# Kernel tuning notes

Hardware: AMD Instinct MI355X
Metric: run time of the kernel (lower is better)

The kernel has to match this reference:

```python
import jax, jax.numpy as jnp
import numpy as np

IN_FEATURES = 512
OUT_FEATURES = 64
INTER = 16
BATCH = 512


def setup_inputs() -> dict:
    key = jax.random.key(0)
    kx, kt = jax.random.split(key)
    x = jax.random.normal(kx, (BATCH, IN_FEATURES), dtype=jnp.float32)
    T = jax.random.normal(kt, (IN_FEATURES, OUT_FEATURES * INTER), dtype=jnp.float32)
    return {"x": x, "T": T}


def reference(x, T):
    B = x.shape[0]
    # M: [B, out, inter]
    M = (x @ T).reshape(B, OUT_FEATURES, INTER)
    # pairwise L1 distance over the intermediate dim: [B, B, out]
    l1 = jnp.sum(jnp.abs(M[:, None, :, :] - M[None, :, :, :]), axis=3)
    sim = jnp.exp(-l1)
    mask = 1.0 - jnp.eye(B, dtype=x.dtype)[:, :, None]  # exclude self
    o_b = jnp.sum(sim * mask, axis=1)  # [B, out]
    return jnp.concatenate([x, o_b], axis=1)
```

## Files before the change

kernel.cpp:

```cpp
#include <hip/hip_runtime.h>

#define OUT_STRIDE 576

typedef __attribute__((ext_vector_type(8))) short bf16x8;
typedef __attribute__((ext_vector_type(4))) float f32x4;

__device__ inline unsigned short f2bf(float f) {
    unsigned u = __float_as_uint(f);
    u = (u + 0x7FFFu + ((u >> 16) & 1u)) >> 16;
    return (unsigned short)u;
}

__global__ __launch_bounds__(256) void transpose_T_kernel(
    const float* __restrict__ T, unsigned short* __restrict__ Tb)
{
    __shared__ float tt[64][68];
    const int b = blockIdx.x;
    const int t = threadIdx.x;
    const int k0 = (b & 7) * 64, n0 = (b >> 3) * 64;
    const int n4 = (t & 15) * 4, kr = t >> 4;
#pragma unroll
    for (int rr = 0; rr < 4; ++rr) {
        const int k = rr * 16 + kr;
        *(float4*)&tt[k][n4] = *(const float4*)(T + (size_t)(k0 + k) * 1024 + n0 + n4);
    }
    __syncthreads();
#pragma unroll
    for (int q = 0; q < 4; ++q) {
        const int g = q * 256 + t;
        const int nn = g >> 4, c = g & 15;
        ushort4 w;
        w.x = f2bf(tt[c * 4 + 0][nn]);
        w.y = f2bf(tt[c * 4 + 1][nn]);
        w.z = f2bf(tt[c * 4 + 2][nn]);
        w.w = f2bf(tt[c * 4 + 3][nn]);
        *(ushort4*)(Tb + (size_t)(n0 + nn) * 512 + k0 + c * 4) = w;
    }
}

__global__ __launch_bounds__(256) void gemm_kernel(
    const float* __restrict__ x, const unsigned short* __restrict__ Tb,
    float* __restrict__ M, float* __restrict__ out)
{
    __shared__ unsigned short As[32 * 72];
    __shared__ unsigned short Bs[64 * 72];
    const int t = threadIdx.x;
    const int bx = blockIdx.x & 15, by = blockIdx.x >> 4;
    const int c0 = bx * 64, r0 = by * 32;
    const int lane = t & 63, w = t >> 6;
    const int m0 = (w >> 1) * 16, nb = (w & 1) * 32;
    const int fl = lane & 15, q8 = (lane >> 4) * 8;
    const int arow = t >> 3, k8 = (t & 7) * 8;

    f32x4 acc0 = {0.f, 0.f, 0.f, 0.f}, acc1 = {0.f, 0.f, 0.f, 0.f};

    for (int kc = 0; kc < 512; kc += 64) {
        {
            const float4 u = *(const float4*)(x + (size_t)(r0 + arow) * 512 + kc + k8);
            const float4 v = *(const float4*)(x + (size_t)(r0 + arow) * 512 + kc + k8 + 4);
            ushort4 w0, w1;
            w0.x = f2bf(u.x); w0.y = f2bf(u.y); w0.z = f2bf(u.z); w0.w = f2bf(u.w);
            w1.x = f2bf(v.x); w1.y = f2bf(v.y); w1.z = f2bf(v.z); w1.w = f2bf(v.w);
            *(ushort4*)&As[arow * 72 + k8] = w0;
            *(ushort4*)&As[arow * 72 + k8 + 4] = w1;
        }
#pragma unroll
        for (int h = 0; h < 2; ++h) {
            const int n = arow + h * 32;
            *(uint4*)&Bs[n * 72 + k8] =
                *(const uint4*)(Tb + (size_t)(c0 + n) * 512 + kc + k8);
        }
        __syncthreads();
        const bf16x8 a0  = *(const bf16x8*)&As[(m0 + fl) * 72 + q8];
        const bf16x8 a1  = *(const bf16x8*)&As[(m0 + fl) * 72 + 32 + q8];
        const bf16x8 b00 = *(const bf16x8*)&Bs[(nb + fl) * 72 + q8];
        const bf16x8 b01 = *(const bf16x8*)&Bs[(nb + fl) * 72 + 32 + q8];
        const bf16x8 b10 = *(const bf16x8*)&Bs[(nb + 16 + fl) * 72 + q8];
        const bf16x8 b11 = *(const bf16x8*)&Bs[(nb + 16 + fl) * 72 + 32 + q8];
        acc0 = __builtin_amdgcn_mfma_f32_16x16x32_bf16(a0, b00, acc0, 0, 0, 0);
        acc0 = __builtin_amdgcn_mfma_f32_16x16x32_bf16(a1, b01, acc0, 0, 0, 0);
        acc1 = __builtin_amdgcn_mfma_f32_16x16x32_bf16(a0, b10, acc1, 0, 0, 0);
        acc1 = __builtin_amdgcn_mfma_f32_16x16x32_bf16(a1, b11, acc1, 0, 0, 0);
        __syncthreads();
    }
    const int orow = r0 + m0 + (lane >> 4) * 4;
#pragma unroll
    for (int r = 0; r < 4; ++r) {
        M[(size_t)(orow + r) * 1024 + c0 + nb + fl]      = acc0[r];
        M[(size_t)(orow + r) * 1024 + c0 + nb + 16 + fl] = acc1[r];
    }

    const int bid = blockIdx.x;
    {
        const int idx = (bid * 256 + t) * 4;
        const int i = idx >> 9, c = idx & 511;
        *(float4*)(out + (size_t)i * OUT_STRIDE + c) = *(const float4*)(x + idx);
    }
    if (t < 128) {
        const int idx = bid * 128 + t;
        const int i = idx >> 6, o = idx & 63;
        out[(size_t)i * OUT_STRIDE + 512 + o] = -1.0f;
    }
}

__global__ __launch_bounds__(256, 4) void pairwise_kernel(
    const float* __restrict__ M, float* __restrict__ out)
{
    __shared__ float sj[8 * 1280];
    const int t = threadIdx.x;
    const int o = t & 63, ig = t >> 6;
    const int it = blockIdx.x & 31, jc = blockIdx.x >> 5;
    const int i0 = it * 16, j0 = jc * 16;

    float mi[4][16];
#pragma unroll
    for (int r = 0; r < 4; ++r) {
        const float* rp = M + (size_t)(i0 + ig * 4 + r) * 1024 + o * 16;
#pragma unroll
        for (int q = 0; q < 4; ++q) {
            const float4 v = *(const float4*)(rp + q * 4);
            mi[r][q * 4 + 0] = v.x; mi[r][q * 4 + 1] = v.y;
            mi[r][q * 4 + 2] = v.z; mi[r][q * 4 + 3] = v.w;
        }
    }
    float acc[4] = {0.f, 0.f, 0.f, 0.f};

    const int os = t >> 2, k4 = t & 3;
#pragma unroll
    for (int jb = 0; jb < 16; jb += 8) {
#pragma unroll
        for (int q = 0; q < 8; ++q) {
            const float4 v = *(const float4*)(M + (size_t)(j0 + jb + q) * 1024 + t * 4);
            *(float4*)&sj[q * 1280 + os * 20 + k4 * 4] = v;
        }
        __syncthreads();
#pragma unroll
        for (int q = 0; q < 8; ++q) {
            const float* s = sj + q * 1280 + o * 20;
            float l1[4] = {0.f, 0.f, 0.f, 0.f};
#pragma unroll
            for (int q4 = 0; q4 < 4; ++q4) {
                const float4 v = *(const float4*)(s + q4 * 4);
#pragma unroll
                for (int r = 0; r < 4; ++r) {
                    l1[r] += fabsf(mi[r][q4 * 4 + 0] - v.x);
                    l1[r] += fabsf(mi[r][q4 * 4 + 1] - v.y);
                    l1[r] += fabsf(mi[r][q4 * 4 + 2] - v.z);
                    l1[r] += fabsf(mi[r][q4 * 4 + 3] - v.w);
                }
            }
#pragma unroll
            for (int r = 0; r < 4; ++r) acc[r] += __expf(-l1[r]);
        }
        __syncthreads();
    }
#pragma unroll
    for (int r = 0; r < 4; ++r)
        atomicAdd(out + (size_t)(i0 + ig * 4 + r) * OUT_STRIDE + 512 + o, acc[r]);
}

extern "C" void kernel_launch(void* const* d_in, const int* in_sizes, int n_in,
                              void* d_out, int out_size, void* d_ws, size_t ws_size,
                              hipStream_t stream) {
    const float* x = (const float*)d_in[0];
    const float* T = (const float*)d_in[1];
    float* out = (float*)d_out;
    float* M = (float*)d_ws;
    unsigned short* Tb = (unsigned short*)((char*)d_ws + (2 << 20));

    transpose_T_kernel<<<128, 256, 0, stream>>>(T, Tb);
    gemm_kernel<<<256, 256, 0, stream>>>(x, Tb, M, out);
    pairwise_kernel<<<1024, 256, 0, stream>>>(M, out);
}
```

Before: 83.86 us.

## Exploit L1 distance symmetry in pairwise kernel; split GEMM into smaller tiles

The pairwise kernel now visits only upper-triangular tile pairs (528 instead of 1024 blocks), mapping the block id to (ti,tj) with a sqrt-based triangular index. Each off-diagonal block also accumulates column sums and scatters them to the j rows through a shared-memory reduction and atomics, which roughly halves the exp and L1 work. In exchange it adds register pressure (16 extra accumulators, occupancy hint lowered from 4 to 3), an extra reduction pass and more atomics. The GEMM moves to 16-row tiles with twice as many blocks to spread work across more CUs.

Result: no change. 83.96 us (+0.1%).

```diff
diff --git a/kernel.cpp b/kernel.cpp
--- a/kernel.cpp
+++ b/kernel.cpp
@@ -42,75 +42,73 @@
     const float* __restrict__ x, const unsigned short* __restrict__ Tb,
     float* __restrict__ M, float* __restrict__ out)
 {
-    __shared__ unsigned short As[32 * 72];
+    __shared__ unsigned short As[16 * 72];
     __shared__ unsigned short Bs[64 * 72];
     const int t = threadIdx.x;
     const int bx = blockIdx.x & 15, by = blockIdx.x >> 4;
-    const int c0 = bx * 64, r0 = by * 32;
+    const int c0 = bx * 64, r0 = by * 16;
     const int lane = t & 63, w = t >> 6;
-    const int m0 = (w >> 1) * 16, nb = (w & 1) * 32;
+    const int nb = w * 16;
     const int fl = lane & 15, q8 = (lane >> 4) * 8;
-    const int arow = t >> 3, k8 = (t & 7) * 8;
+    const int ar = t >> 4, ak4 = (t & 15) * 4;
+    const int bn = t >> 3, bk8 = (t & 7) * 8;
 
-    f32x4 acc0 = {0.f, 0.f, 0.f, 0.f}, acc1 = {0.f, 0.f, 0.f, 0.f};
+    f32x4 acc = {0.f, 0.f, 0.f, 0.f};
 
     for (int kc = 0; kc < 512; kc += 64) {
         {
-            const float4 u = *(const float4*)(x + (size_t)(r0 + arow) * 512 + kc + k8);
-            const float4 v = *(const float4*)(x + (size_t)(r0 + arow) * 512 + kc + k8 + 4);
-            ushort4 w0, w1;
+            const float4 u = *(const float4*)(x + (size_t)(r0 + ar) * 512 + kc + ak4);
+            ushort4 w0;
             w0.x = f2bf(u.x); w0.y = f2bf(u.y); w0.z = f2bf(u.z); w0.w = f2bf(u.w);
-            w1.x = f2bf(v.x); w1.y = f2bf(v.y); w1.z = f2bf(v.z); w1.w = f2bf(v.w);
-            *(ushort4*)&As[arow * 72 + k8] = w0;
-            *(ushort4*)&As[arow * 72 + k8 + 4] = w1;
+            *(ushort4*)&As[ar * 72 + ak4] = w0;
         }
 #pragma unroll
         for (int h = 0; h < 2; ++h) {
-            const int n = arow + h * 32;
-            *(uint4*)&Bs[n * 72 + k8] =
-                *(const uint4*)(Tb + (size_t)(c0 + n) * 512 + kc + k8);
+            const int n = bn + h * 32;
+            *(uint4*)&Bs[n * 72 + bk8] =
+                *(const uint4*)(Tb + (size_t)(c0 + n) * 512 + kc + bk8);
         }
         __syncthreads();
-        const bf16x8 a0  = *(const bf16x8*)&As[(m0 + fl) * 72 + q8];
-        const bf16x8 a1  = *(const bf16x8*)&As[(m0 + fl) * 72 + 32 + q8];
-        const bf16x8 b00 = *(const bf16x8*)&Bs[(nb + fl) * 72 + q8];
-        const bf16x8 b01 = *(const bf16x8*)&Bs[(nb + fl) * 72 + 32 + q8];
-        const bf16x8 b10 = *(const bf16x8*)&Bs[(nb + 16 + fl) * 72 + q8];
-        const bf16x8 b11 = *(const bf16x8*)&Bs[(nb + 16 + fl) * 72 + 32 + q8];
-        acc0 = __builtin_amdgcn_mfma_f32_16x16x32_bf16(a0, b00, acc0, 0, 0, 0);
-        acc0 = __builtin_amdgcn_mfma_f32_16x16x32_bf16(a1, b01, acc0, 0, 0, 0);
-        acc1 = __builtin_amdgcn_mfma_f32_16x16x32_bf16(a0, b10, acc1, 0, 0, 0);
-        acc1 = __builtin_amdgcn_mfma_f32_16x16x32_bf16(a1, b11, acc1, 0, 0, 0);
+        const bf16x8 a0 = *(const bf16x8*)&As[fl * 72 + q8];
+        const bf16x8 a1 = *(const bf16x8*)&As[fl * 72 + 32 + q8];
+        const bf16x8 b0 = *(const bf16x8*)&Bs[(nb + fl) * 72 + q8];
+        const bf16x8 b1 = *(const bf16x8*)&Bs[(nb + fl) * 72 + 32 + q8];
+        acc = __builtin_amdgcn_mfma_f32_16x16x32_bf16(a0, b0, acc, 0, 0, 0);
+        acc = __builtin_amdgcn_mfma_f32_16x16x32_bf16(a1, b1, acc, 0, 0, 0);
         __syncthreads();
     }
-    const int orow = r0 + m0 + (lane >> 4) * 4;
+    const int orow = r0 + (lane >> 4) * 4;
 #pragma unroll
-    for (int r = 0; r < 4; ++r) {
-        M[(size_t)(orow + r) * 1024 + c0 + nb + fl]      = acc0[r];
-        M[(size_t)(orow + r) * 1024 + c0 + nb + 16 + fl] = acc1[r];
-    }
+    for (int r = 0; r < 4; ++r)
+        M[(size_t)(orow + r) * 1024 + c0 + nb + fl] = acc[r];
 
     const int bid = blockIdx.x;
-    {
-        const int idx = (bid * 256 + t) * 4;
+    if (t < 128) {
+        const int idx = (bid * 128 + t) * 4;
         const int i = idx >> 9, c = idx & 511;
         *(float4*)(out + (size_t)i * OUT_STRIDE + c) = *(const float4*)(x + idx);
-    }
-    if (t < 128) {
-        const int idx = bid * 128 + t;
+    } else if (t < 192) {
+        const int idx = bid * 64 + (t - 128);
         const int i = idx >> 6, o = idx & 63;
         out[(size_t)i * OUT_STRIDE + 512 + o] = -1.0f;
     }
 }
 
-__global__ __launch_bounds__(256, 4) void pairwise_kernel(
+__global__ __launch_bounds__(256, 3) void pairwise_kernel(
     const float* __restrict__ M, float* __restrict__ out)
 {
     __shared__ float sj[8 * 1280];
     const int t = threadIdx.x;
     const int o = t & 63, ig = t >> 6;
-    const int it = blockIdx.x & 31, jc = blockIdx.x >> 5;
-    const int i0 = it * 16, j0 = jc * 16;
+    const int b = blockIdx.x;
+
+    int ti = (int)((65.0f - sqrtf(4225.0f - 8.0f * (float)b)) * 0.5f);
+    if (b < ti * (65 - ti) / 2) --ti;
+    else if (b >= (ti + 1) * (64 - ti) / 2) ++ti;
+    const int st = ti * (65 - ti) / 2;
+    const int tj = ti + (b - st);
+    const int i0 = ti * 16, j0 = tj * 16;
+    const bool diag = (ti == tj);
 
     float mi[4][16];
 #pragma unroll
@@ -123,7 +121,10 @@
             mi[r][q * 4 + 2] = v.z; mi[r][q * 4 + 3] = v.w;
         }
     }
-    float acc[4] = {0.f, 0.f, 0.f, 0.f};
+    float acci[4] = {0.f, 0.f, 0.f, 0.f};
+    float accj[16];
+#pragma unroll
+    for (int j = 0; j < 16; ++j) accj[j] = 0.f;
 
     const int os = t >> 2, k4 = t & 3;
 #pragma unroll
@@ -149,14 +150,31 @@
                     l1[r] += fabsf(mi[r][q4 * 4 + 3] - v.w);
                 }
             }
-#pragma unroll
-            for (int r = 0; r < 4; ++r) acc[r] += __expf(-l1[r]);
+            float e0 = __expf(-l1[0]), e1 = __expf(-l1[1]);
+            float e2 = __expf(-l1[2]), e3 = __expf(-l1[3]);
+            acci[0] += e0; acci[1] += e1; acci[2] += e2; acci[3] += e3;
+            if (!diag) accj[jb + q] += (e0 + e1) + (e2 + e3);
         }
         __syncthreads();
     }
+
 #pragma unroll
     for (int r = 0; r < 4; ++r)
-        atomicAdd(out + (size_t)(i0 + ig * 4 + r) * OUT_STRIDE + 512 + o, acc[r]);
+        atomicAdd(out + (size_t)(i0 + ig * 4 + r) * OUT_STRIDE + 512 + o, acci[r]);
+
+    if (!diag) {
+#pragma unroll
+        for (int j = 0; j < 16; ++j)
+            sj[ig * 1024 + j * 64 + o] = accj[j];
+        __syncthreads();
+#pragma unroll
+        for (int p = 0; p < 4; ++p) {
+            const int jj = ig * 4 + p;
+            const float s = sj[0 * 1024 + jj * 64 + o] + sj[1 * 1024 + jj * 64 + o]
+                          + sj[2 * 1024 + jj * 64 + o] + sj[3 * 1024 + jj * 64 + o];
+            atomicAdd(out + (size_t)(j0 + jj) * OUT_STRIDE + 512 + o, s);
+        }
+    }
 }
 
 extern "C" void kernel_launch(void* const* d_in, const int* in_sizes, int n_in,
@@ -169,6 +187,6 @@
     unsigned short* Tb = (unsigned short*)((char*)d_ws + (2 << 20));
 
     transpose_T_kernel<<<128, 256, 0, stream>>>(T, Tb);
-    gemm_kernel<<<256, 256, 0, stream>>>(x, Tb, M, out);
-    pairwise_kernel<<<1024, 256, 0, stream>>>(M, out);
+    gemm_kernel<<<512, 256, 0, stream>>>(x, Tb, M, out);
+    pairwise_kernel<<<528, 256, 0, stream>>>(M, out);
 }
```
